# Kernel optimization log

Hardware: AMD Instinct MI355X
Metric: run time of the kernel (lower is better)

The kernel has to match this reference:

```python
import jax, jax.numpy as jnp
import numpy as np
from jax import lax

WS = 11          # window_size
SIGMA = 1.5
CH = 3
PAD = WS // 2


def _depthwise_conv(x, w, groups):
    # x: [B, C, H, W], w: [C_out, C_in/groups, kh, kw]
    return lax.conv_general_dilated(
        x, w, window_strides=(1, 1), padding=[(PAD, PAD), (PAD, PAD)],
        feature_group_count=groups,
        dimension_numbers=("NCHW", "OIHW", "NCHW"))


def _make_window():
    xs = jnp.arange(WS, dtype=jnp.float32) - (WS // 2)
    g = jnp.exp(-(xs ** 2) / (2.0 * SIGMA ** 2))
    g = g / g.sum()
    w2d = jnp.outer(g, g)                       # [WS, WS]
    return jnp.broadcast_to(w2d, (CH, 1, WS, WS))  # depthwise kernel


def setup_inputs() -> dict:
    key = jax.random.key(0)
    k1, k2, k3 = jax.random.split(key, 3)
    B, H, W = 16, 512, 512
    img1 = jax.random.uniform(k1, (B, CH, H, W), dtype=jnp.float32)
    img2 = jax.random.uniform(k2, (B, CH, H, W), dtype=jnp.float32)
    match = jax.random.uniform(k3, (B, 1, H, W), dtype=jnp.float32)
    return {"img1": img1, "img2": img2, "match": match}


def reference(img1, img2, match):
    window = _make_window()
    box = jnp.ones((1, 1, WS, WS), dtype=jnp.float32) / (WS * WS)

    # mask from match map: box-filter then threshold
    m = _depthwise_conv(match, box, 1) + 1e-07
    mask = (m > 0.5).astype(jnp.float32) + 1e-07   # [B,1,H,W]

    mu1 = _depthwise_conv(img1, window, CH)
    mu2 = _depthwise_conv(img2, window, CH)
    mu1_sq = mu1 * mu1
    mu2_sq = mu2 * mu2
    mu1_mu2 = mu1 * mu2
    sigma1_sq = _depthwise_conv(img1 * img1, window, CH) - mu1_sq
    sigma2_sq = _depthwise_conv(img2 * img2, window, CH) - mu2_sq
    sigma12 = _depthwise_conv(img1 * img2, window, CH) - mu1_mu2

    C1 = 0.01 ** 2
    C2 = 0.03 ** 2
    ssim_map = ((2 * mu1_mu2 + C1) * (2 * sigma12 + C2)) / (
        (mu1_sq + mu2_sq + C1) * (sigma1_sq + sigma2_sq + C2))

    # mask [B,1,H,W] broadcasts over the 3 channels of ssim_map
    return jnp.sum((1.0 - ssim_map) * mask) / jnp.sum(mask) / 3.0
```

## Files before the change

kernel.cpp:

```cpp
#include <hip/hip_runtime.h>


#define BATCH 16
#define CHANS 3
#define IMH 512
#define IMW 512
#define STRIPW 64
#define STRIPH 256
#define RINGR 18
#define LDSW 84
#define SUP 8
#define NSUP (STRIPH / SUP)
#define NQ 20

__device__ __forceinline__ float4 ld4s(const float* p) { return *(const float4*)p; }
__device__ __forceinline__ void st4s(float* p, float4 v) { *(float4*)p = v; }
__device__ __forceinline__ void fma4(float4& a, float w, float4 x) {
    a.x = fmaf(w, x.x, a.x); a.y = fmaf(w, x.y, a.y);
    a.z = fmaf(w, x.z, a.z); a.w = fmaf(w, x.w, a.w);
}
__device__ __forceinline__ void fma4m(float4& a, float w, float4 x, float4 y) {
    a.x = fmaf(w, x.x * y.x, a.x); a.y = fmaf(w, x.y * y.y, a.y);
    a.z = fmaf(w, x.z * y.z, a.z); a.w = fmaf(w, x.w * y.w, a.w);
}
__device__ __forceinline__ void add4(float4& a, float4 x) {
    a.x += x.x; a.y += x.y; a.z += x.z; a.w += x.w;
}

__device__ __forceinline__ void convg(const float* __restrict__ row, int cb,
                                      const float* __restrict__ g, float out[4]) {
    float w[20];
    #pragma unroll
    for (int i = 0; i < 5; ++i) {
        float4 v = ld4s(row + cb + 4 * i);
        w[4*i+0] = v.x; w[4*i+1] = v.y; w[4*i+2] = v.z; w[4*i+3] = v.w;
    }
    #pragma unroll
    for (int j = 0; j < 4; ++j) {
        float a = 0.0f;
        #pragma unroll
        for (int k = 0; k < 11; ++k) a = fmaf(g[k], w[3 + j + k], a);
        out[j] = a;
    }
}

__device__ __forceinline__ void convb(const float* __restrict__ row, int cb,
                                      float out[4]) {
    float w[20];
    #pragma unroll
    for (int i = 0; i < 5; ++i) {
        float4 v = ld4s(row + cb + 4 * i);
        w[4*i+0] = v.x; w[4*i+1] = v.y; w[4*i+2] = v.z; w[4*i+3] = v.w;
    }
    #pragma unroll
    for (int j = 0; j < 4; ++j) {
        float a = 0.0f;
        #pragma unroll
        for (int k = 0; k < 11; ++k) a += w[3 + j + k];
        out[j] = a;
    }
}

__global__ __launch_bounds__(256) void ssim_main(
    const float* __restrict__ img1, const float* __restrict__ img2,
    const float* __restrict__ match, double* __restrict__ acc)
{
    __shared__ __align__(16) float ring1[RINGR][LDSW];
    __shared__ __align__(16) float ring2[RINGR][LDSW];
    __shared__ __align__(16) float ringm[RINGR][LDSW];
    __shared__ __align__(16) float fld[6][SUP][LDSW];
    __shared__ float redn[4], redd[4];

    const int tid = threadIdx.x;
    const int bc = blockIdx.z;
    const int b = bc / CHANS;
    const int c = bc - b * CHANS;
    const int ystart = blockIdx.y * STRIPH;
    const int bx0 = blockIdx.x * STRIPW - 8;

    const float* p1 = img1 + (size_t)(b * CHANS + c) * (IMH * IMW);
    const float* p2 = img2 + (size_t)(b * CHANS + c) * (IMH * IMW);
    const float* pm = match + (size_t)b * (IMH * IMW);

    float g[11];
    {
        float s = 0.0f;
        #pragma unroll
        for (int i = 0; i < 11; ++i) {
            float d = (float)(i - 5);
            g[i] = expf(-(d * d) / 4.5f);
            s += g[i];
        }
        #pragma unroll
        for (int i = 0; i < 11; ++i) g[i] /= s;
    }

    float num = 0.0f, den = 0.0f;

    auto stage = [&](int gy0, int nrows) {
        for (int t = tid; t < nrows * NQ; t += 256) {
            int r = t / NQ, q = t - r * NQ;
            int gy = gy0 + r;
            int slot = (gy + 36) % RINGR;
            int gx = bx0 + 4 * q;
            float4 v1, v2, vm;
            if ((unsigned)gy < IMH && (unsigned)gx <= (IMW - 4)) {
                const float* base = p1 + gy * IMW + gx;
                v1 = ld4s(base);
                v2 = ld4s(p2 + gy * IMW + gx);
                vm = ld4s(pm + gy * IMW + gx);
            } else if ((unsigned)gy < IMH) {
                float t1[4], t2[4], tm[4];
                #pragma unroll
                for (int e = 0; e < 4; ++e) {
                    int x = gx + e;
                    bool ok = (unsigned)x < IMW;
                    int off = gy * IMW + (ok ? x : 0);
                    t1[e] = ok ? p1[off] : 0.0f;
                    t2[e] = ok ? p2[off] : 0.0f;
                    tm[e] = ok ? pm[off] : 0.0f;
                }
                v1 = make_float4(t1[0], t1[1], t1[2], t1[3]);
                v2 = make_float4(t2[0], t2[1], t2[2], t2[3]);
                vm = make_float4(tm[0], tm[1], tm[2], tm[3]);
            } else {
                v1 = v2 = vm = make_float4(0.f, 0.f, 0.f, 0.f);
            }
            st4s(&ring1[slot][4 * q], v1);
            st4s(&ring2[slot][4 * q], v2);
            st4s(&ringm[slot][4 * q], vm);
        }
    };

    stage(ystart - 5, 10);

    for (int s = 0; s < NSUP; ++s) {
        const int ybase = ystart + s * SUP;

        stage(ybase + 5, SUP);
        __syncthreads();

        if (tid < SUP * NQ) {
            int r = tid / NQ, q = tid - r * NQ;
            int cq = 4 * q;
            int y = ybase + r;
            int sr = (y - 5 + 36) % RINGR;
            float4 a1 = make_float4(0,0,0,0), a2 = a1, a3 = a1,
                   a4 = a1, a5 = a1, am = a1;
            #pragma unroll
            for (int k = 0; k < 11; ++k) {
                float4 x1 = ld4s(&ring1[sr][cq]);
                float4 x2 = ld4s(&ring2[sr][cq]);
                float4 xm = ld4s(&ringm[sr][cq]);
                float w = g[k];
                fma4(a1, w, x1);
                fma4(a2, w, x2);
                fma4m(a3, w, x1, x1);
                fma4m(a4, w, x2, x2);
                fma4m(a5, w, x1, x2);
                add4(am, xm);
                sr++; if (sr >= RINGR) sr -= RINGR;
            }
            st4s(&fld[0][r][cq], a1);
            st4s(&fld[1][r][cq], a2);
            st4s(&fld[2][r][cq], a3);
            st4s(&fld[3][r][cq], a4);
            st4s(&fld[4][r][cq], a5);
            st4s(&fld[5][r][cq], am);
        }
        __syncthreads();

        if (tid < SUP * 16) {
            int r = tid >> 4, q = tid & 15;
            int cb = 4 * q;
            float mu1[4], mu2[4], m11[4], m22[4], m12[4], mb[4];
            convg(fld[0][r], cb, g, mu1);
            convg(fld[1][r], cb, g, mu2);
            convg(fld[2][r], cb, g, m11);
            convg(fld[3][r], cb, g, m22);
            convg(fld[4][r], cb, g, m12);
            convb(fld[5][r], cb, mb);
            #pragma unroll
            for (int j = 0; j < 4; ++j) {
                float mu1s = mu1[j] * mu1[j];
                float mu2s = mu2[j] * mu2[j];
                float mu12 = mu1[j] * mu2[j];
                float sg1  = m11[j] - mu1s;
                float sg2  = m22[j] - mu2s;
                float sg12 = m12[j] - mu12;
                float ssim = ((2.0f * mu12 + 1e-4f) * (2.0f * sg12 + 9e-4f)) /
                             ((mu1s + mu2s + 1e-4f) * (sg1 + sg2 + 9e-4f));
                float m = mb[j] * (1.0f / 121.0f) + 1e-7f;
                float mask = (m > 0.5f) ? (1.0f + 1e-7f) : 1e-7f;
                num += (1.0f - ssim) * mask;
                den += mask;
            }
        }
    }

    for (int off = 32; off > 0; off >>= 1) {
        num += __shfl_down(num, off);
        den += __shfl_down(den, off);
    }
    int wave = tid >> 6;
    int lane = tid & 63;
    if (lane == 0) { redn[wave] = num; redd[wave] = den; }
    __syncthreads();
    if (tid == 0) {
        float n = redn[0] + redn[1] + redn[2] + redn[3];
        atomicAdd(&acc[0], (double)n);
        if (c == 0) {
            float d = redd[0] + redd[1] + redd[2] + redd[3];
            atomicAdd(&acc[1], (double)d);
        }
    }
}

__global__ void init_acc(double* acc) {
    acc[0] = 0.0;
    acc[1] = 0.0;
}

__global__ void finalize(const double* __restrict__ acc, float* __restrict__ out) {
    out[0] = (float)(acc[0] / acc[1] / 3.0);
}

extern "C" void kernel_launch(void* const* d_in, const int* in_sizes, int n_in,
                              void* d_out, int out_size, void* d_ws, size_t ws_size,
                              hipStream_t stream) {
    const float* img1  = (const float*)d_in[0];
    const float* img2  = (const float*)d_in[1];
    const float* match = (const float*)d_in[2];
    float* out = (float*)d_out;
    double* acc = (double*)d_ws;

    init_acc<<<1, 1, 0, stream>>>(acc);

    dim3 grid(IMW / STRIPW, IMH / STRIPH, BATCH * CHANS);
    dim3 block(256, 1, 1);
    ssim_main<<<grid, block, 0, stream>>>(img1, img2, match, acc);

    finalize<<<1, 1, 0, stream>>>(acc, out);
}
```

Baseline: 246.5 us.

## Precompute binary mask once per batch image and halve strip height

Adds a separate mask_pass kernel that box-filters the match map once per batch image and writes a byte mask to workspace, along with the mask denominator. The main SSIM kernel then reads the byte mask instead of staging and filtering the match map three times (once per channel), which removes a third LDS ring and its loads. Strip height is halved to launch more blocks, and launch bounds request higher occupancy. In exchange it adds a kernel launch, a round trip of the mask through global memory, and more halo rows recomputed because strips are shorter. A fallback path keeps the old kernel when the workspace is too small.

```diff
diff --git a/kernel.cpp b/kernel.cpp
--- a/kernel.cpp
+++ b/kernel.cpp
@@ -6,12 +6,16 @@
 #define IMH 512
 #define IMW 512
 #define STRIPW 64
-#define STRIPH 256
+#define STRIPH 128
 #define RINGR 18
 #define LDSW 84
 #define SUP 8
 #define NSUP (STRIPH / SUP)
 #define NQ 20
+
+#define MTW 64
+#define MTH 64
+#define MRAWH 74
 
 __device__ __forceinline__ float4 ld4s(const float* p) { return *(const float4*)p; }
 __device__ __forceinline__ void st4s(float* p, float4 v) { *(float4*)p = v; }
@@ -61,7 +65,218 @@
     }
 }
 
-__global__ __launch_bounds__(256) void ssim_main(
+__global__ __launch_bounds__(256) void mask_pass(
+    const float* __restrict__ match, unsigned char* __restrict__ maskbuf,
+    double* __restrict__ acc)
+{
+    __shared__ __align__(16) float raw[MRAWH][LDSW];
+    __shared__ __align__(16) float vs[MTH][LDSW];
+    __shared__ float red[4];
+
+    const int tid = threadIdx.x;
+    const int b = blockIdx.z;
+    const int x0 = blockIdx.x * MTW - 8;
+    const int y0 = blockIdx.y * MTH - 5;
+    const float* pm = match + (size_t)b * (IMH * IMW);
+
+    for (int t = tid; t < MRAWH * NQ; t += 256) {
+        int r = t / NQ, q = t - r * NQ;
+        int gy = y0 + r;
+        int gx = x0 + 4 * q;
+        float4 v = make_float4(0.f, 0.f, 0.f, 0.f);
+        if ((unsigned)gy < IMH) {
+            if ((unsigned)gx <= (IMW - 4)) {
+                v = ld4s(pm + gy * IMW + gx);
+            } else {
+                float tmp[4];
+                #pragma unroll
+                for (int e = 0; e < 4; ++e) {
+                    int x = gx + e;
+                    bool ok = (unsigned)x < IMW;
+                    tmp[e] = ok ? pm[gy * IMW + x] : 0.0f;
+                }
+                v = make_float4(tmp[0], tmp[1], tmp[2], tmp[3]);
+            }
+        }
+        st4s(&raw[r][4 * q], v);
+    }
+    __syncthreads();
+
+    for (int t = tid; t < MTH * NQ; t += 256) {
+        int r = t / NQ, q = t - r * NQ;
+        int cq = 4 * q;
+        float4 a = make_float4(0.f, 0.f, 0.f, 0.f);
+        #pragma unroll
+        for (int k = 0; k < 11; ++k) add4(a, ld4s(&raw[r + k][cq]));
+        st4s(&vs[r][cq], a);
+    }
+    __syncthreads();
+
+    float den = 0.0f;
+    for (int t = tid; t < MTH * 16; t += 256) {
+        int r = t >> 4, q = t & 15;
+        float mb[4];
+        convb(vs[r], 4 * q, mb);
+        unsigned char bits[4];
+        #pragma unroll
+        for (int j = 0; j < 4; ++j) {
+            float m = mb[j] * (1.0f / 121.0f) + 1e-7f;
+            bool on = m > 0.5f;
+            bits[j] = (unsigned char)on;
+            den += on ? (1.0f + 1e-7f) : 1e-7f;
+        }
+        int gy = blockIdx.y * MTH + r;
+        int gx = blockIdx.x * MTW + 4 * q;
+        *(uchar4*)(maskbuf + ((size_t)b << 18) + (gy << 9) + gx) =
+            make_uchar4(bits[0], bits[1], bits[2], bits[3]);
+    }
+
+    for (int off = 32; off > 0; off >>= 1) den += __shfl_down(den, off);
+    if ((tid & 63) == 0) red[tid >> 6] = den;
+    __syncthreads();
+    if (tid == 0)
+        atomicAdd(&acc[1], (double)(red[0] + red[1] + red[2] + red[3]));
+}
+
+__global__ __launch_bounds__(256, 6) void ssim_main_pm(
+    const float* __restrict__ img1, const float* __restrict__ img2,
+    const unsigned char* __restrict__ maskbuf, double* __restrict__ acc)
+{
+    __shared__ __align__(16) float ring1[RINGR][LDSW];
+    __shared__ __align__(16) float ring2[RINGR][LDSW];
+    __shared__ __align__(16) float fld[5][SUP][LDSW];
+    __shared__ float redn[4];
+
+    const int tid = threadIdx.x;
+    const int bc = blockIdx.z;
+    const int b = bc / CHANS;
+    const int c = bc - b * CHANS;
+    const int ystart = blockIdx.y * STRIPH;
+    const int bxg = blockIdx.x;
+    const int bx0 = bxg * STRIPW - 8;
+
+    const float* p1 = img1 + (size_t)(b * CHANS + c) * (IMH * IMW);
+    const float* p2 = img2 + (size_t)(b * CHANS + c) * (IMH * IMW);
+    const unsigned char* pmk = maskbuf + ((size_t)b << 18);
+
+    float g[11];
+    {
+        float s = 0.0f;
+        #pragma unroll
+        for (int i = 0; i < 11; ++i) {
+            float d = (float)(i - 5);
+            g[i] = expf(-(d * d) / 4.5f);
+            s += g[i];
+        }
+        #pragma unroll
+        for (int i = 0; i < 11; ++i) g[i] /= s;
+    }
+
+    float num = 0.0f;
+    const bool colsafe = (bx0 >= 0) && (bx0 + 4 * NQ <= IMW);
+
+    auto stage = [&](int gy0, int nrows) {
+        if (tid < nrows * NQ) {
+            int r = tid / NQ, q = tid - r * NQ;
+            int gy = gy0 + r;
+            int slot = (gy + 36) % RINGR;
+            int gx = bx0 + 4 * q;
+            float4 v1 = make_float4(0.f, 0.f, 0.f, 0.f), v2 = v1;
+            if ((unsigned)gy < IMH) {
+                if (colsafe || (unsigned)gx <= (IMW - 4)) {
+                    v1 = ld4s(p1 + gy * IMW + gx);
+                    v2 = ld4s(p2 + gy * IMW + gx);
+                } else {
+                    float t1[4], t2[4];
+                    #pragma unroll
+                    for (int e = 0; e < 4; ++e) {
+                        int x = gx + e;
+                        bool ok = (unsigned)x < IMW;
+                        int off = gy * IMW + (ok ? x : 0);
+                        t1[e] = ok ? p1[off] : 0.0f;
+                        t2[e] = ok ? p2[off] : 0.0f;
+                    }
+                    v1 = make_float4(t1[0], t1[1], t1[2], t1[3]);
+                    v2 = make_float4(t2[0], t2[1], t2[2], t2[3]);
+                }
+            }
+            st4s(&ring1[slot][4 * q], v1);
+            st4s(&ring2[slot][4 * q], v2);
+        }
+    };
+
+    stage(ystart - 5, 10);
+
+    for (int s = 0; s < NSUP; ++s) {
+        const int ybase = ystart + s * SUP;
+
+        stage(ybase + 5, SUP);
+        __syncthreads();
+
+        if (tid < SUP * NQ) {
+            int r = tid / NQ, q = tid - r * NQ;
+            int cq = 4 * q;
+            int sr = (ybase + r + 31) % RINGR;
+            float4 a1 = make_float4(0,0,0,0), a2 = a1, a3 = a1,
+                   a4 = a1, a5 = a1;
+            #pragma unroll
+            for (int k = 0; k < 11; ++k) {
+                float4 x1 = ld4s(&ring1[sr][cq]);
+                float4 x2 = ld4s(&ring2[sr][cq]);
+                float w = g[k];
+                fma4(a1, w, x1);
+                fma4(a2, w, x2);
+                fma4m(a3, w, x1, x1);
+                fma4m(a4, w, x2, x2);
+                fma4m(a5, w, x1, x2);
+                sr++; if (sr >= RINGR) sr -= RINGR;
+            }
+            st4s(&fld[0][r][cq], a1);
+            st4s(&fld[1][r][cq], a2);
+            st4s(&fld[2][r][cq], a3);
+            st4s(&fld[3][r][cq], a4);
+            st4s(&fld[4][r][cq], a5);
+        }
+        __syncthreads();
+
+        if (tid < SUP * 16) {
+            int r = tid >> 4, q = tid & 15;
+            int cb = 4 * q;
+            float mu1[4], mu2[4], m11[4], m22[4], m12[4];
+            convg(fld[0][r], cb, g, mu1);
+            convg(fld[1][r], cb, g, mu2);
+            convg(fld[2][r], cb, g, m11);
+            convg(fld[3][r], cb, g, m22);
+            convg(fld[4][r], cb, g, m12);
+            int gy = ybase + r;
+            int gx = bxg * STRIPW + cb;
+            uchar4 mk = *(const uchar4*)(pmk + (gy << 9) + gx);
+            const unsigned char mkv[4] = {mk.x, mk.y, mk.z, mk.w};
+            #pragma unroll
+            for (int j = 0; j < 4; ++j) {
+                float mu1s = mu1[j] * mu1[j];
+                float mu2s = mu2[j] * mu2[j];
+                float mu12 = mu1[j] * mu2[j];
+                float sg1  = m11[j] - mu1s;
+                float sg2  = m22[j] - mu2s;
+                float sg12 = m12[j] - mu12;
+                float ssim = ((2.0f * mu12 + 1e-4f) * (2.0f * sg12 + 9e-4f)) /
+                             ((mu1s + mu2s + 1e-4f) * (sg1 + sg2 + 9e-4f));
+                float mask = mkv[j] ? (1.0f + 1e-7f) : 1e-7f;
+                num += (1.0f - ssim) * mask;
+            }
+        }
+    }
+
+    for (int off = 32; off > 0; off >>= 1) num += __shfl_down(num, off);
+    if ((tid & 63) == 0) redn[tid >> 6] = num;
+    __syncthreads();
+    if (tid == 0)
+        atomicAdd(&acc[0], (double)(redn[0] + redn[1] + redn[2] + redn[3]));
+    (void)c;
+}
+
+__global__ __launch_bounds__(256) void ssim_main_fb(
     const float* __restrict__ img1, const float* __restrict__ img2,
     const float* __restrict__ match, double* __restrict__ acc)
 {
@@ -105,8 +320,7 @@
             int gx = bx0 + 4 * q;
             float4 v1, v2, vm;
             if ((unsigned)gy < IMH && (unsigned)gx <= (IMW - 4)) {
-                const float* base = p1 + gy * IMW + gx;
-                v1 = ld4s(base);
+                v1 = ld4s(p1 + gy * IMW + gx);
                 v2 = ld4s(p2 + gy * IMW + gx);
                 vm = ld4s(pm + gy * IMW + gx);
             } else if ((unsigned)gy < IMH) {
@@ -136,15 +350,13 @@
 
     for (int s = 0; s < NSUP; ++s) {
         const int ybase = ystart + s * SUP;
-
         stage(ybase + 5, SUP);
         __syncthreads();
 
         if (tid < SUP * NQ) {
             int r = tid / NQ, q = tid - r * NQ;
             int cq = 4 * q;
-            int y = ybase + r;
-            int sr = (y - 5 + 36) % RINGR;
+            int sr = (ybase + r + 31) % RINGR;
             float4 a1 = make_float4(0,0,0,0), a2 = a1, a3 = a1,
                    a4 = a1, a5 = a1, am = a1;
             #pragma unroll
@@ -236,9 +448,18 @@
 
     init_acc<<<1, 1, 0, stream>>>(acc);
 
-    dim3 grid(IMW / STRIPW, IMH / STRIPH, BATCH * CHANS);
+    const size_t mask_need = 64 + (size_t)BATCH * IMH * IMW;
     dim3 block(256, 1, 1);
-    ssim_main<<<grid, block, 0, stream>>>(img1, img2, match, acc);
+    if (ws_size >= mask_need) {
+        unsigned char* mbuf = (unsigned char*)d_ws + 64;
+        dim3 mgrid(IMW / MTW, IMH / MTH, BATCH);
+        mask_pass<<<mgrid, block, 0, stream>>>(match, mbuf, acc);
+        dim3 grid(IMW / STRIPW, IMH / STRIPH, BATCH * CHANS);
+        ssim_main_pm<<<grid, block, 0, stream>>>(img1, img2, mbuf, acc);
+    } else {
+        dim3 grid(IMW / STRIPW, IMH / STRIPH, BATCH * CHANS);
+        ssim_main_fb<<<grid, block, 0, stream>>>(img1, img2, match, acc);
+    }
 
     finalize<<<1, 1, 0, stream>>>(acc, out);
 }
```

Result: slower. 591.1 us (+139.8%).
